# Kernel tuning notes

Measured on AMD Instinct MI355X. Metric: run time of the kernel, lower is better.

The kernel has to match this reference:

```python
import jax, jax.numpy as jnp
import numpy as np

L = 2048          # seq len
DIM = 1024        # model dim
NL = 12           # num layers
VOCAB = 50257
PAD_VOCAB = 50264 # vocab padded to multiple of 8 for embedding
N = 16            # ssm state dim
K = 4             # conv kernel size
E = 2048          # d_inner = expand * dim
DTR = 64          # dt_rank = ceil(dim/16)
EPS = 1e-5


def setup_inputs() -> dict:
    key = jax.random.key(0)
    ks = jax.random.split(key, 12)
    s = 0.02
    f32 = jnp.float32
    # HiPPO-style A init: A_log = log(1..N) broadcast over channels
    A_log = jnp.log(jnp.broadcast_to(jnp.arange(1, N + 1, dtype=f32), (NL, E, N)))
    return {
        "input_ids": jax.random.randint(ks[0], (L,), 0, VOCAB),
        "embed": jax.random.normal(ks[1], (PAD_VOCAB, DIM), f32) * s,
        "in_proj_w": jax.random.normal(ks[2], (NL, 2 * E, DIM), f32) * s,
        "conv_w": jax.random.normal(ks[3], (NL, E, K), f32) * s,
        "conv_b": jnp.zeros((NL, E), f32),
        "x_proj_w": jax.random.normal(ks[4], (NL, DTR + 2 * N, E), f32) * s,
        "dt_proj_w": jax.random.normal(ks[5], (NL, E, DTR), f32) * s,
        "dt_proj_b": jax.random.normal(ks[6], (NL, E), f32) * 0.1,
        "A_log": A_log,
        "D_param": jnp.ones((NL, E), f32),
        "out_proj_w": jax.random.normal(ks[7], (NL, DIM, E), f32) * s,
        "norm_w": jnp.ones((NL, DIM), f32),
        "norm_f_w": jnp.ones((DIM,), f32),
        "head_w": jax.random.normal(ks[8], (VOCAB, DIM), f32) * s,
    }


def rmsnorm(x, w):
    # per-token RMSNorm over last axis (matches eqx.nn.RMSNorm vmapped per token)
    inv = jax.lax.rsqrt(jnp.mean(x * x, axis=-1, keepdims=True) + EPS)
    return x * inv * w


def causal_dw_conv(x, w, b):
    # x: [L, E], w: [E, K] depthwise causal conv, b: [E]
    out = jax.lax.conv_general_dilated(
        x.T[None],            # [1, E, L]
        w[:, None, :],        # [E, 1, K]
        (1,), [(K - 1, 0)],
        feature_group_count=E,
        dimension_numbers=("NCH", "OIH", "NCH"),
    )
    return out[0].T + b       # [L, E]


def mamba_block(x, in_w, cw, cb, xp_w, dt_w, dt_b, A_log, D, out_w):
    # x: [L, DIM]
    xz = x @ in_w.T                       # [L, 2E]
    xi, z = xz[:, :E], xz[:, E:]
    xc = jax.nn.silu(causal_dw_conv(xi, cw, cb))   # [L, E]
    dbc = xc @ xp_w.T                     # [L, DTR + 2N]
    dt = jax.nn.softplus(dbc[:, :DTR] @ dt_w.T + dt_b)  # [L, E]
    B = dbc[:, DTR:DTR + N]               # [L, N]
    C = dbc[:, DTR + N:]                  # [L, N]
    A = -jnp.exp(A_log)                   # [E, N]
    dA = jnp.exp(dt[:, :, None] * A)                       # [L, E, N]
    dBu = dt[:, :, None] * B[:, None, :] * xc[:, :, None]  # [L, E, N]

    def step(h, inp):
        dA_t, dBu_t = inp
        h = dA_t * h + dBu_t
        return h, h

    _, hs = jax.lax.scan(step, jnp.zeros((E, N), x.dtype), (dA, dBu))
    y = jnp.einsum("len,ln->le", hs, C) + D * xc
    y = y * jax.nn.silu(z)
    return y @ out_w.T                    # [L, DIM]


def reference(input_ids, embed, in_proj_w, conv_w, conv_b, x_proj_w,
              dt_proj_w, dt_proj_b, A_log, D_param, out_proj_w,
              norm_w, norm_f_w, head_w):
    x = embed[input_ids]                  # [L, DIM]
    res = None
    for i in range(NL):
        res = x + res if res is not None else x
        h = rmsnorm(res, norm_w[i])
        x = mamba_block(h, in_proj_w[i], conv_w[i], conv_b[i], x_proj_w[i],
                        dt_proj_w[i], dt_proj_b[i], A_log[i], D_param[i],
                        out_proj_w[i])
    res = x + res
    x = rmsnorm(res, norm_f_w)
    return x @ head_w.T                   # [L, VOCAB]
```

## Files before the change

### kernel.cpp

```cpp
#include <hip/hip_runtime.h>
#include <math.h>

#define LSEQ 2048
#define DMODEL 1024
#define NLAYER 12
#define NVOCAB 50257
#define NPADV 50304
#define EDIM 2048
#define NST 16
#define DTRANK 64
#define EPSV 1e-5f
#define NCHUNK 64
#define TCHUNK 32

typedef __attribute__((ext_vector_type(4))) float float4v;
typedef __attribute__((ext_vector_type(8))) short short8v;
typedef __attribute__((ext_vector_type(4))) unsigned short ushort4v;
typedef unsigned short u16;

__device__ __forceinline__ u16 f2bf(float f) {
    union { float f; unsigned int u; } v; v.f = f;
    unsigned int r = v.u + 0x7FFFu + ((v.u >> 16) & 1u);
    return (u16)(r >> 16);
}

__device__ __forceinline__ ushort4v cvt4(float4 a) {
    ushort4v r; r[0] = f2bf(a.x); r[1] = f2bf(a.y); r[2] = f2bf(a.z); r[3] = f2bf(a.w);
    return r;
}

__device__ __forceinline__ float4v mfma_bf16(short8v a, short8v b, float4v c) {
    return __builtin_amdgcn_mfma_f32_16x16x32_bf16(a, b, c, 0, 0, 0);
}

__device__ __forceinline__ void gload_lds16(const void* g, void* l) {
    __builtin_amdgcn_global_load_lds(
        (const __attribute__((address_space(1))) unsigned int*)g,
        (__attribute__((address_space(3))) unsigned int*)l,
        16, 0, 0);
}

__global__ __launch_bounds__(256) void k_embed(const int* __restrict__ ids,
                                               const float* __restrict__ emb,
                                               float* __restrict__ res) {
    const int t = blockIdx.x;
    const int row = ids[t];
    ((float4*)(res + (size_t)t * DMODEL))[threadIdx.x] =
        ((const float4*)(emb + (size_t)row * DMODEL))[threadIdx.x];
}

template<bool ADD>
__global__ __launch_bounds__(256) void k_addnorm(float* __restrict__ res,
                                                 const float* __restrict__ xin,
                                                 const float* __restrict__ w,
                                                 u16* __restrict__ h) {
    const int t = blockIdx.x;
    const int i = threadIdx.x;
    float4 r = ((float4*)(res + (size_t)t * DMODEL))[i];
    if (ADD) {
        float4 xv = ((const float4*)(xin + (size_t)t * DMODEL))[i];
        r.x += xv.x; r.y += xv.y; r.z += xv.z; r.w += xv.w;
        ((float4*)(res + (size_t)t * DMODEL))[i] = r;
    }
    float ss = r.x * r.x + r.y * r.y + r.z * r.z + r.w * r.w;
#pragma unroll
    for (int off = 32; off > 0; off >>= 1) ss += __shfl_xor(ss, off);
    __shared__ float part[4];
    if ((i & 63) == 0) part[i >> 6] = ss;
    __syncthreads();
    float tot = part[0] + part[1] + part[2] + part[3];
    const float inv = rsqrtf(tot * (1.f / DMODEL) + EPSV);
    float4 wv = ((const float4*)w)[i];
    float4 o;
    o.x = r.x * inv * wv.x; o.y = r.y * inv * wv.y;
    o.z = r.z * inv * wv.z; o.w = r.w * inv * wv.w;
    ((ushort4v*)(h + (size_t)t * DMODEL))[i] = cvt4(o);
}

__global__ __launch_bounds__(256) void k_cvt(const float* __restrict__ s, u16* __restrict__ d,
                                             long long n, long long ntot) {
    const long long stride = (long long)gridDim.x * 256 * 8;
    for (long long i = ((long long)blockIdx.x * 256 + threadIdx.x) * 8; i < ntot; i += stride) {
        ushort4v lo, hi;
        if (i < n) {
            float4 a = *(const float4*)(s + i);
            float4 b = *(const float4*)(s + i + 4);
            lo = cvt4(a); hi = cvt4(b);
        } else {
            lo[0] = lo[1] = lo[2] = lo[3] = 0;
            hi[0] = hi[1] = hi[2] = hi[3] = 0;
        }
        *(ushort4v*)(d + i) = lo;
        *(ushort4v*)(d + i + 4) = hi;
    }
}

__global__ __launch_bounds__(256) void k_cvtL(const float* __restrict__ sa, u16* __restrict__ da, long long na,
                                              const float* __restrict__ sb, u16* __restrict__ db, long long nb,
                                              const float* __restrict__ sc, u16* __restrict__ dc, long long nc,
                                              const float* __restrict__ sd, u16* __restrict__ dd, long long nd) {
    const long long tot = na + nb + nc + nd;
    const long long stride = (long long)gridDim.x * 256 * 8;
    for (long long i = ((long long)blockIdx.x * 256 + threadIdx.x) * 8; i < tot; i += stride) {
        const float* s; u16* d; long long o = i;
        if (o < na) { s = sa; d = da; }
        else { o -= na;
            if (o < nb) { s = sb; d = db; }
            else { o -= nb;
                if (o < nc) { s = sc; d = dc; }
                else { o -= nc; s = sd; d = dd; } } }
        float4 a = *(const float4*)(s + o);
        float4 b = *(const float4*)(s + o + 4);
        *(ushort4v*)(d + o) = cvt4(a);
        *(ushort4v*)(d + o + 4) = cvt4(b);
    }
}

template<int MT, int EPI, bool NTS>
__global__ __launch_bounds__(256, 4) void k_gemm128(const u16* __restrict__ A,
                                                    const u16* __restrict__ W,
                                                    float* __restrict__ C,
                                                    const float* __restrict__ bias,
                                                    int N, int K, int ldc, int cpx) {
    __shared__ __align__(128) u16 lds[2][8192];
    const int tid = threadIdx.x;
    const int w = tid >> 6;
    const int lane = tid & 63;
    const int l16 = lane & 15;
    const int quad = lane >> 4;
    const int wm = (w >> 1) * 64;
    const int wn = (w & 1) * 64;
    const int bid = blockIdx.x;
    const int orig = (bid & 7) * cpx + (bid >> 3);
    const int bm = orig & (MT - 1);
    const int bn = orig / MT;
    const int row0 = bm * 128, col0 = bn * 128;

    const int scol = ((lane & 3) ^ ((lane >> 3) & 3)) * 8;
    const int lrow = lane >> 2;
    const u16* sbase[4];
#pragma unroll
    for (int c = 0; c < 4; ++c) {
        const int g = w * 4 + c;
        sbase[c] = (g < 8 ? A + (size_t)(row0 + g * 16 + lrow) * K
                          : W + (size_t)(col0 + (g - 8) * 16 + lrow) * K) + scol;
    }

    const int swz = (quad ^ ((l16 >> 1) & 3)) * 8;
    const int aoff = (wm + l16) * 32 + swz;
    const int boff = 4096 + (wn + l16) * 32 + swz;

    float4v acc[4][4];
#pragma unroll
    for (int i = 0; i < 4; ++i)
#pragma unroll
        for (int j = 0; j < 4; ++j)
#pragma unroll
            for (int r = 0; r < 4; ++r) acc[i][j][r] = 0.f;

    const int NT = K >> 5;

    auto stage_tile = [&](int buf, int t) {
#pragma unroll
        for (int c = 0; c < 4; ++c)
            gload_lds16(sbase[c] + t * 32, &lds[buf][(w * 4 + c) * 512]);
    };

    stage_tile(0, 0);
    stage_tile(1, 1);
    asm volatile("s_waitcnt vmcnt(4)" ::: "memory");
    __builtin_amdgcn_s_barrier();

    for (int n = 0; n < NT; ++n) {
        const u16* Ls = &lds[n & 1][0];
        short8v af[4], bf[4];
#pragma unroll
        for (int ii = 0; ii < 4; ++ii)
            af[ii] = *(const short8v*)&Ls[aoff + ii * 512];
#pragma unroll
        for (int j = 0; j < 4; ++j)
            bf[j] = *(const short8v*)&Ls[boff + j * 512];
        __builtin_amdgcn_s_barrier();
        __builtin_amdgcn_s_setprio(1);
#pragma unroll
        for (int ii = 0; ii < 4; ++ii)
#pragma unroll
            for (int j = 0; j < 4; ++j)
                acc[ii][j] = mfma_bf16(af[ii], bf[j], acc[ii][j]);
        __builtin_amdgcn_s_setprio(0);
        if (n + 2 < NT) {
            stage_tile(n & 1, n + 2);
            asm volatile("s_waitcnt vmcnt(4)" ::: "memory");
        } else if (n < NT - 1) {
            asm volatile("s_waitcnt vmcnt(0)" ::: "memory");
        }
        __builtin_amdgcn_s_barrier();
    }

    float* lt = (float*)(&lds[0][0]) + (size_t)w * 1040;
    const int ecol = col0 + wn + lane;
    float bv = 0.f;
    if (EPI == 1) bv = bias[(ecol < N) ? ecol : 0];
#pragma unroll
    for (int i = 0; i < 4; ++i) {
        __syncthreads();
#pragma unroll
        for (int j = 0; j < 4; ++j)
#pragma unroll
            for (int r = 0; r < 4; ++r)
                lt[(quad * 4 + r) * 65 + j * 16 + l16] = acc[i][j][r];
        __syncthreads();
        if (ecol < N) {
            const int rbase = row0 + wm + i * 16;
#pragma unroll
            for (int t = 0; t < 16; ++t) {
                float v = lt[t * 65 + lane];
                if (EPI == 1) { v += bv; v = (v > 20.f) ? v : log1pf(__expf(v)); }
                float* p = &C[(size_t)(rbase + t) * ldc + ecol];
                if (NTS) __builtin_nontemporal_store(v, p);
                else *p = v;
            }
        }
    }
}

template<int TM, int TN>
__global__ __launch_bounds__(256) void k_gemm_bf(const u16* __restrict__ A,
                                                 const u16* __restrict__ W,
                                                 float* __restrict__ C,
                                                 int N, int K, int ldc) {
    constexpr int NI = TM / 32, NJ = TN / 32, CA = TM / 64, CB = TN / 64;
    __shared__ u16 As[TM * 32];
    __shared__ u16 Bs[TN * 32];
    __shared__ float lt_s[4][16 * 33];
    const int tid = threadIdx.x;
    const int lane = tid & 63;
    const int wave = tid >> 6;
    const int l16 = lane & 15;
    const int quad = lane >> 4;
    const int wm = (wave >> 1) * (TM / 2);
    const int wn = (wave & 1) * (TN / 2);
    const int srow = lane >> 2;
    const int scol = ((lane & 3) ^ ((lane >> 3) & 3)) * 8;
    const int bm = blockIdx.x, bn = blockIdx.y;

    const u16* Ab = A + ((size_t)bm * TM + srow) * K + scol;
    const u16* Wb = W + ((size_t)bn * TN + srow) * K + scol;

    const int qs = (quad ^ ((l16 >> 1) & 3)) * 8;

    float4v acc[NI][NJ];
#pragma unroll
    for (int i = 0; i < NI; ++i)
#pragma unroll
        for (int j = 0; j < NJ; ++j)
#pragma unroll
            for (int r = 0; r < 4; ++r) acc[i][j][r] = 0.f;

    for (int k0 = 0; k0 < K; k0 += 32) {
#pragma unroll
        for (int c = 0; c < CA; ++c) {
            const int chunk = wave * CA + c;
            gload_lds16(Ab + (size_t)chunk * 16 * K + k0, &As[chunk * 512]);
        }
#pragma unroll
        for (int c = 0; c < CB; ++c) {
            const int chunk = wave * CB + c;
            gload_lds16(Wb + (size_t)chunk * 16 * K + k0, &Bs[chunk * 512]);
        }
        __syncthreads();
        short8v af[NI], bfr[NJ];
#pragma unroll
        for (int i = 0; i < NI; ++i)
            af[i] = *(const short8v*)&As[(wm + i * 16 + l16) * 32 + qs];
#pragma unroll
        for (int j = 0; j < NJ; ++j)
            bfr[j] = *(const short8v*)&Bs[(wn + j * 16 + l16) * 32 + qs];
#pragma unroll
        for (int i = 0; i < NI; ++i)
#pragma unroll
            for (int j = 0; j < NJ; ++j)
                acc[i][j] = mfma_bf16(af[i], bfr[j], acc[i][j]);
        __syncthreads();
    }

    float* lt = &lt_s[wave][0];
    const int c32 = lane & 31;
    const int rsub = lane >> 5;
    const int ecol = bn * TN + wn + c32;
#pragma unroll
    for (int i = 0; i < NI; ++i) {
        __syncthreads();
#pragma unroll
        for (int j = 0; j < NJ; ++j)
#pragma unroll
            for (int r = 0; r < 4; ++r)
                lt[(quad * 4 + r) * 33 + j * 16 + l16] = acc[i][j][r];
        __syncthreads();
        if (ecol < N) {
            const int rbase = bm * TM + wm + i * 16;
#pragma unroll
            for (int t = 0; t < 8; ++t)
                C[(size_t)(rbase + 2 * t + rsub) * ldc + ecol] =
                    lt[(2 * t + rsub) * 33 + c32];
        }
    }
}

__global__ __launch_bounds__(256) void k_conv(const float* __restrict__ xz,
                                              const float* __restrict__ cw,
                                              const float* __restrict__ cb,
                                              float* __restrict__ xc,
                                              u16* __restrict__ xc16) {
    const int e = blockIdx.x * 256 + threadIdx.x;
    const int t0 = blockIdx.y * 8;
    const float w0 = cw[e * 4 + 0], w1 = cw[e * 4 + 1], w2 = cw[e * 4 + 2], w3 = cw[e * 4 + 3];
    const float b = cb[e];
    float xm3 = (t0 >= 3) ? xz[(size_t)(t0 - 3) * (2 * EDIM) + e] : 0.f;
    float xm2 = (t0 >= 2) ? xz[(size_t)(t0 - 2) * (2 * EDIM) + e] : 0.f;
    float xm1 = (t0 >= 1) ? xz[(size_t)(t0 - 1) * (2 * EDIM) + e] : 0.f;
#pragma unroll
    for (int s = 0; s < 8; ++s) {
        const int t = t0 + s;
        const float xt = xz[(size_t)t * (2 * EDIM) + e];
        const float v = w0 * xm3 + w1 * xm2 + w2 * xm1 + w3 * xt + b;
        const float sv = v / (1.f + __expf(-v));
        xc[(size_t)t * EDIM + e] = sv;
        xc16[(size_t)t * EDIM + e] = f2bf(sv);
        xm3 = xm2; xm2 = xm1; xm1 = xt;
    }
}

__global__ __launch_bounds__(256) void k_xproj(const u16* __restrict__ xc,
                                               const u16* __restrict__ W,
                                               float* __restrict__ dbc,
                                               u16* __restrict__ dbc16) {
    const int tid = threadIdx.x;
    const int wave = tid >> 6, lane = tid & 63;
    const int l16 = lane & 15, quad = lane >> 4;
    const int m = blockIdx.x * 16 + l16;
    const int kb = wave * (EDIM / 4);
    float4v acc[6];
#pragma unroll
    for (int j = 0; j < 6; ++j)
#pragma unroll
        for (int r = 0; r < 4; ++r) acc[j][r] = 0.f;

    for (int ks = 0; ks < EDIM / 4; ks += 32) {
        const int k = kb + ks + quad * 8;
        const short8v af = *(const short8v*)(xc + (size_t)m * EDIM + k);
#pragma unroll
        for (int j = 0; j < 6; ++j) {
            const short8v bf = *(const short8v*)(W + (size_t)(j * 16 + l16) * EDIM + k);
            acc[j] = mfma_bf16(af, bf, acc[j]);
        }
    }
    __shared__ float red[4][16][96];
#pragma unroll
    for (int j = 0; j < 6; ++j)
#pragma unroll
        for (int r = 0; r < 4; ++r)
            red[wave][quad * 4 + r][j * 16 + l16] = acc[j][r];
    __syncthreads();
    for (int idx = tid; idx < 16 * 96; idx += 256) {
        const int r = idx / 96, c = idx % 96;
        const float s = red[0][r][c] + red[1][r][c] + red[2][r][c] + red[3][r][c];
        const int row = blockIdx.x * 16 + r;
        dbc[(size_t)row * 96 + c] = s;
        if (c < 64) dbc16[(size_t)row * 64 + c] = f2bf(s);
    }
}

__global__ __launch_bounds__(256) void k_scanA(const float* __restrict__ dt,
                                               const float* __restrict__ xc,
                                               const float* __restrict__ dbc,
                                               const float* __restrict__ Al,
                                               float* __restrict__ hpart,
                                               float* __restrict__ sdtb) {
    const int e = blockIdx.y * 256 + threadIdx.x;
    const int c = blockIdx.x;
    float a[NST];
#pragma unroll
    for (int n = 0; n < NST; ++n) a[n] = -__expf(Al[(size_t)e * NST + n]);
    bool fast = true;
#pragma unroll
    for (int n = 0; n < NST; ++n)
        fast = fast && (fabsf(a[n] + (float)(n + 1)) < 1e-3f * (float)(n + 1));
    __align__(16) float h[NST];
#pragma unroll
    for (int n = 0; n < NST; ++n) h[n] = 0.f;
    float sdt = 0.f;
    const int t0 = c * TCHUNK;
    if (fast) {
        for (int s = 0; s < TCHUNK; ++s) {
            const int t = t0 + s;
            const float d = dt[(size_t)t * EDIM + e];
            const float x = xc[(size_t)t * EDIM + e];
            __align__(16) float Bv[NST];
#pragma unroll
            for (int q = 0; q < 4; ++q)
                *(float4*)&Bv[q * 4] = *(const float4*)&dbc[(size_t)t * 96 + 64 + q * 4];
            const float u = d * x;
            sdt += d;
            const float d1 = __expf(-d);
            float pw = 1.f;
#pragma unroll
            for (int n = 0; n < NST; ++n) { pw *= d1; h[n] = fmaf(pw, h[n], u * Bv[n]); }
        }
    } else {
        for (int s = 0; s < TCHUNK; ++s) {
            const int t = t0 + s;
            const float d = dt[(size_t)t * EDIM + e];
            const float x = xc[(size_t)t * EDIM + e];
            __align__(16) float Bv[NST];
#pragma unroll
            for (int q = 0; q < 4; ++q)
                *(float4*)&Bv[q * 4] = *(const float4*)&dbc[(size_t)t * 96 + 64 + q * 4];
            const float u = d * x;
            sdt += d;
#pragma unroll
            for (int n = 0; n < NST; ++n) h[n] = fmaf(__expf(d * a[n]), h[n], u * Bv[n]);
        }
    }
#pragma unroll
    for (int n = 0; n < NST; n += 4)
        *(float4*)&hpart[((size_t)c * EDIM + e) * NST + n] = *(float4*)&h[n];
    sdtb[(size_t)c * EDIM + e] = sdt;
}

__global__ __launch_bounds__(256) void k_scanB(float* __restrict__ hio,
                                               const float* __restrict__ sdtb,
                                               const float* __restrict__ Al) {
    const int idx = blockIdx.x * 256 + threadIdx.x;
    const int e = idx >> 4;
    const float a = -__expf(Al[idx]);
    float carry = 0.f;
    for (int c = 0; c < NCHUNK; ++c) {
        const size_t off = ((size_t)c * EDIM + e) * NST + (idx & 15);
        const float hp = hio[off];
        const float ap = __expf(a * sdtb[(size_t)c * EDIM + e]);
        hio[off] = carry;
        carry = fmaf(ap, carry, hp);
    }
}

__global__ __launch_bounds__(256) void k_scanC(const float* __restrict__ dt,
                                               const float* __restrict__ xc,
                                               const float* __restrict__ dbc,
                                               const float* __restrict__ xz,
                                               const float* __restrict__ Al,
                                               const float* __restrict__ Dl,
                                               const float* __restrict__ hin,
                                               u16* __restrict__ y) {
    const int e = blockIdx.y * 256 + threadIdx.x;
    const int c = blockIdx.x;
    float a[NST];
#pragma unroll
    for (int n = 0; n < NST; ++n) a[n] = -__expf(Al[(size_t)e * NST + n]);
    bool fast = true;
#pragma unroll
    for (int n = 0; n < NST; ++n)
        fast = fast && (fabsf(a[n] + (float)(n + 1)) < 1e-3f * (float)(n + 1));
    __align__(16) float h[NST];
#pragma unroll
    for (int n = 0; n < NST; n += 4)
        *(float4*)&h[n] = *(const float4*)&hin[((size_t)c * EDIM + e) * NST + n];
    const float Dv = Dl[e];
    const int t0 = c * TCHUNK;
    for (int s = 0; s < TCHUNK; ++s) {
        const int t = t0 + s;
        const float d = dt[(size_t)t * EDIM + e];
        const float x = xc[(size_t)t * EDIM + e];
        __align__(16) float Bv[NST], Cv[NST];
#pragma unroll
        for (int q = 0; q < 4; ++q) {
            *(float4*)&Bv[q * 4] = *(const float4*)&dbc[(size_t)t * 96 + 64 + q * 4];
            *(float4*)&Cv[q * 4] = *(const float4*)&dbc[(size_t)t * 96 + 80 + q * 4];
        }
        const float u = d * x;
        float ys = 0.f;
        if (fast) {
            const float d1 = __expf(-d);
            float pw = 1.f;
#pragma unroll
            for (int n = 0; n < NST; ++n) {
                pw *= d1;
                h[n] = fmaf(pw, h[n], u * Bv[n]);
                ys = fmaf(h[n], Cv[n], ys);
            }
        } else {
#pragma unroll
            for (int n = 0; n < NST; ++n) {
                h[n] = fmaf(__expf(d * a[n]), h[n], u * Bv[n]);
                ys = fmaf(h[n], Cv[n], ys);
            }
        }
        const float z = xz[(size_t)t * (2 * EDIM) + EDIM + e];
        const float yv = ys + Dv * x;
        y[(size_t)t * EDIM + e] = f2bf(yv * (z / (1.f + __expf(-z))));
    }
}

extern "C" void kernel_launch(void* const* d_in, const int* in_sizes, int n_in,
                              void* d_out, int out_size, void* d_ws, size_t ws_size,
                              hipStream_t stream) {
    const int*   ids   = (const int*)d_in[0];
    const float* emb   = (const float*)d_in[1];
    const float* inW   = (const float*)d_in[2];
    const float* convW = (const float*)d_in[3];
    const float* convB = (const float*)d_in[4];
    const float* xpW   = (const float*)d_in[5];
    const float* dtW   = (const float*)d_in[6];
    const float* dtB   = (const float*)d_in[7];
    const float* Alog  = (const float*)d_in[8];
    const float* Dpar  = (const float*)d_in[9];
    const float* outW  = (const float*)d_in[10];
    const float* normW = (const float*)d_in[11];
    const float* normF = (const float*)d_in[12];
    const float* headW = (const float*)d_in[13];
    float* out = (float*)d_out;

    float* ws    = (float*)d_ws;
    float* res   = ws;
    float* xzb   = res   + (size_t)LSEQ * DMODEL;
    float* xcb   = xzb   + (size_t)LSEQ * 2 * EDIM;
    float* dbcb  = xcb   + (size_t)LSEQ * EDIM;
    float* dtb   = dbcb  + (size_t)LSEQ * 96;
    float* xob   = dtb   + (size_t)LSEQ * EDIM;
    float* hpart = xob   + (size_t)LSEQ * DMODEL;
    float* sdtb  = hpart + (size_t)NCHUNK * EDIM * NST;
    u16* hbf  = (u16*)(sdtb + (size_t)NCHUNK * EDIM);
    u16* ybf  = hbf  + (size_t)LSEQ * DMODEL;
    u16* wbf  = ybf  + (size_t)LSEQ * EDIM;
    u16* wbf2 = wbf  + (size_t)2 * EDIM * DMODEL;
    u16* xc16  = wbf  + (size_t)12 * 1024 * 1024;
    u16* dbc16 = xc16 + (size_t)LSEQ * EDIM;
    u16* xpw16 = dbc16 + (size_t)LSEQ * DTRANK;
    u16* dtw16 = xpw16 + (size_t)96 * EDIM;

    k_embed<<<LSEQ, 256, 0, stream>>>(ids, emb, res);

    for (int i = 0; i < NLAYER; ++i) {
        if (i == 0)
            k_addnorm<false><<<LSEQ, 256, 0, stream>>>(res, nullptr, normW, hbf);
        else
            k_addnorm<true><<<LSEQ, 256, 0, stream>>>(res, xob, normW + (size_t)i * DMODEL, hbf);

        k_cvtL<<<4096, 256, 0, stream>>>(
            inW  + (size_t)i * 2 * EDIM * DMODEL, wbf,   (long long)2 * EDIM * DMODEL,
            outW + (size_t)i * DMODEL * EDIM,     wbf2,  (long long)DMODEL * EDIM,
            xpW  + (size_t)i * 96 * EDIM,         xpw16, (long long)96 * EDIM,
            dtW  + (size_t)i * EDIM * DTRANK,     dtw16, (long long)EDIM * DTRANK);

        k_gemm128<16, 0, false><<<dim3(512), 256, 0, stream>>>(hbf, wbf, xzb, nullptr,
                2 * EDIM, DMODEL, 2 * EDIM, 64);

        k_conv<<<dim3(8, 256), 256, 0, stream>>>(xzb, convW + (size_t)i * EDIM * 4,
                convB + (size_t)i * EDIM, xcb, xc16);

        k_xproj<<<128, 256, 0, stream>>>(xc16, xpw16, dbcb, dbc16);

        k_gemm128<16, 1, false><<<dim3(256), 256, 0, stream>>>(dbc16, dtw16, dtb,
                dtB + (size_t)i * EDIM, EDIM, DTRANK, EDIM, 32);

        const float* Al = Alog + (size_t)i * EDIM * NST;
        k_scanA<<<dim3(NCHUNK, EDIM / 256), 256, 0, stream>>>(dtb, xcb, dbcb, Al, hpart, sdtb);
        k_scanB<<<(EDIM * NST) / 256, 256, 0, stream>>>(hpart, sdtb, Al);
        k_scanC<<<dim3(NCHUNK, EDIM / 256), 256, 0, stream>>>(dtb, xcb, dbcb, xzb, Al,
                Dpar + (size_t)i * EDIM, hpart, ybf);

        k_gemm_bf<64, 64><<<dim3(32, 16), 256, 0, stream>>>(ybf, wbf2, xob,
                DMODEL, EDIM, DMODEL);
    }

    k_addnorm<true><<<LSEQ, 256, 0, stream>>>(res, xob, normF, hbf);

    k_cvt<<<4096, 256, 0, stream>>>(headW, wbf,
            (long long)NVOCAB * DMODEL, (long long)NPADV * DMODEL);
    k_gemm128<16, 0, true><<<dim3(6288), 256, 0, stream>>>(hbf, wbf, out, nullptr,
            NVOCAB, DMODEL, NVOCAB, 6288 / 8);
}
```

Measured before the change: 2.981 ms.

## Triple-buffer LDS in 128-tile GEMM and pipeline out_proj with 64-tile kernel

```diff
diff --git a/kernel.cpp b/kernel.cpp
--- a/kernel.cpp
+++ b/kernel.cpp
@@ -117,12 +117,12 @@
 }
 
 template<int MT, int EPI, bool NTS>
-__global__ __launch_bounds__(256, 4) void k_gemm128(const u16* __restrict__ A,
+__global__ __launch_bounds__(256, 3) void k_gemm128(const u16* __restrict__ A,
                                                     const u16* __restrict__ W,
                                                     float* __restrict__ C,
                                                     const float* __restrict__ bias,
                                                     int N, int K, int ldc, int cpx) {
-    __shared__ __align__(128) u16 lds[2][8192];
+    __shared__ __align__(128) u16 lds[3][8192];
     const int tid = threadIdx.x;
     const int w = tid >> 6;
     const int lane = tid & 63;
@@ -159,11 +159,13 @@
             for (int r = 0; r < 4; ++r) acc[i][j][r] = 0.f;
 
     const int NT = K >> 5;
+    u16* lds0 = &lds[0][0];
 
     auto stage_tile = [&](int buf, int t) {
+        u16* dst = lds0 + buf * 8192;
 #pragma unroll
         for (int c = 0; c < 4; ++c)
-            gload_lds16(sbase[c] + t * 32, &lds[buf][(w * 4 + c) * 512]);
+            gload_lds16(sbase[c] + t * 32, dst + (w * 4 + c) * 512);
     };
 
     stage_tile(0, 0);
@@ -171,8 +173,9 @@
     asm volatile("s_waitcnt vmcnt(4)" ::: "memory");
     __builtin_amdgcn_s_barrier();
 
+    int cur = 0;
     for (int n = 0; n < NT; ++n) {
-        const u16* Ls = &lds[n & 1][0];
+        const u16* Ls = lds0 + cur * 8192;
         short8v af[4], bf[4];
 #pragma unroll
         for (int ii = 0; ii < 4; ++ii)
@@ -180,7 +183,11 @@
 #pragma unroll
         for (int j = 0; j < 4; ++j)
             bf[j] = *(const short8v*)&Ls[boff + j * 512];
-        __builtin_amdgcn_s_barrier();
+        const bool pf = (n + 2 < NT);
+        if (pf) {
+            int tg = cur + 2; if (tg >= 3) tg -= 3;
+            stage_tile(tg, n + 2);
+        }
         __builtin_amdgcn_s_setprio(1);
 #pragma unroll
         for (int ii = 0; ii < 4; ++ii)
@@ -188,16 +195,15 @@
             for (int j = 0; j < 4; ++j)
                 acc[ii][j] = mfma_bf16(af[ii], bf[j], acc[ii][j]);
         __builtin_amdgcn_s_setprio(0);
-        if (n + 2 < NT) {
-            stage_tile(n & 1, n + 2);
+        if (pf)
             asm volatile("s_waitcnt vmcnt(4)" ::: "memory");
-        } else if (n < NT - 1) {
+        else if (n + 1 < NT)
             asm volatile("s_waitcnt vmcnt(0)" ::: "memory");
-        }
         __builtin_amdgcn_s_barrier();
-    }
-
-    float* lt = (float*)(&lds[0][0]) + (size_t)w * 1040;
+        ++cur; if (cur == 3) cur = 0;
+    }
+
+    float* lt = (float*)lds0 + (size_t)w * 1040;
     const int ecol = col0 + wn + lane;
     float bv = 0.f;
     if (EPI == 1) bv = bias[(ecol < N) ? ecol : 0];
@@ -224,81 +230,116 @@
     }
 }
 
-template<int TM, int TN>
-__global__ __launch_bounds__(256) void k_gemm_bf(const u16* __restrict__ A,
-                                                 const u16* __restrict__ W,
-                                                 float* __restrict__ C,
-                                                 int N, int K, int ldc) {
-    constexpr int NI = TM / 32, NJ = TN / 32, CA = TM / 64, CB = TN / 64;
-    __shared__ u16 As[TM * 32];
-    __shared__ u16 Bs[TN * 32];
-    __shared__ float lt_s[4][16 * 33];
+template<int MT>
+__global__ __launch_bounds__(256, 3) void k_gemm64(const u16* __restrict__ A,
+                                                   const u16* __restrict__ W,
+                                                   float* __restrict__ C,
+                                                   int N, int K, int ldc, int cpx) {
+    __shared__ __align__(128) u16 lds[3][8192];
     const int tid = threadIdx.x;
+    const int w = tid >> 6;
     const int lane = tid & 63;
-    const int wave = tid >> 6;
     const int l16 = lane & 15;
     const int quad = lane >> 4;
-    const int wm = (wave >> 1) * (TM / 2);
-    const int wn = (wave & 1) * (TN / 2);
-    const int srow = lane >> 2;
+    const int wm = (w >> 1) * 32;
+    const int wn = (w & 1) * 32;
+    const int bid = blockIdx.x;
+    const int orig = (bid & 7) * cpx + (bid >> 3);
+    const int bm = orig & (MT - 1);
+    const int bn = orig / MT;
+    const int row0 = bm * 64, col0 = bn * 64;
+
     const int scol = ((lane & 3) ^ ((lane >> 3) & 3)) * 8;
-    const int bm = blockIdx.x, bn = blockIdx.y;
-
-    const u16* Ab = A + ((size_t)bm * TM + srow) * K + scol;
-    const u16* Wb = W + ((size_t)bn * TN + srow) * K + scol;
-
-    const int qs = (quad ^ ((l16 >> 1) & 3)) * 8;
-
-    float4v acc[NI][NJ];
-#pragma unroll
-    for (int i = 0; i < NI; ++i)
-#pragma unroll
-        for (int j = 0; j < NJ; ++j)
+    const int lrow = lane >> 2;
+    const u16* sbase[4];
+#pragma unroll
+    for (int c = 0; c < 4; ++c) {
+        const int ch = w * 4 + c;
+        const int isA = (ch < 8);
+        const int cc = isA ? ch : (ch - 8);
+        const int half = cc >> 2;
+        const int rbase = (cc & 3) * 16;
+        sbase[c] = (isA ? A + (size_t)(row0 + rbase + lrow) * K
+                        : W + (size_t)(col0 + rbase + lrow) * K) + half * 32 + scol;
+    }
+
+    const int swz = (quad ^ ((l16 >> 1) & 3)) * 8;
+    const int aoff = (wm + l16) * 32 + swz;
+    const int boff = 4096 + (wn + l16) * 32 + swz;
+
+    float4v acc[2][2];
+#pragma unroll
+    for (int i = 0; i < 2; ++i)
+#pragma unroll
+        for (int j = 0; j < 2; ++j)
 #pragma unroll
             for (int r = 0; r < 4; ++r) acc[i][j][r] = 0.f;
 
-    for (int k0 = 0; k0 < K; k0 += 32) {
-#pragma unroll
-        for (int c = 0; c < CA; ++c) {
-            const int chunk = wave * CA + c;
-            gload_lds16(Ab + (size_t)chunk * 16 * K + k0, &As[chunk * 512]);
-        }
-#pragma unroll
-        for (int c = 0; c < CB; ++c) {
-            const int chunk = wave * CB + c;
-            gload_lds16(Wb + (size_t)chunk * 16 * K + k0, &Bs[chunk * 512]);
-        }
-        __syncthreads();
-        short8v af[NI], bfr[NJ];
-#pragma unroll
-        for (int i = 0; i < NI; ++i)
-            af[i] = *(const short8v*)&As[(wm + i * 16 + l16) * 32 + qs];
-#pragma unroll
-        for (int j = 0; j < NJ; ++j)
-            bfr[j] = *(const short8v*)&Bs[(wn + j * 16 + l16) * 32 + qs];
-#pragma unroll
-        for (int i = 0; i < NI; ++i)
-#pragma unroll
-            for (int j = 0; j < NJ; ++j)
-                acc[i][j] = mfma_bf16(af[i], bfr[j], acc[i][j]);
-        __syncthreads();
-    }
-
-    float* lt = &lt_s[wave][0];
+    const int NT = K >> 6;
+    u16* lds0 = &lds[0][0];
+
+    auto stage_tile = [&](int buf, int t) {
+        u16* dst = lds0 + buf * 8192;
+#pragma unroll
+        for (int c = 0; c < 4; ++c)
+            gload_lds16(sbase[c] + t * 64, dst + (w * 4 + c) * 512);
+    };
+
+    stage_tile(0, 0);
+    stage_tile(1, 1);
+    asm volatile("s_waitcnt vmcnt(4)" ::: "memory");
+    __builtin_amdgcn_s_barrier();
+
+    int cur = 0;
+    for (int n = 0; n < NT; ++n) {
+        const u16* Ls = lds0 + cur * 8192;
+        short8v af[2][2], bf[2][2];
+#pragma unroll
+        for (int ks = 0; ks < 2; ++ks) {
+#pragma unroll
+            for (int ii = 0; ii < 2; ++ii)
+                af[ks][ii] = *(const short8v*)&Ls[ks * 2048 + aoff + ii * 512];
+#pragma unroll
+            for (int j = 0; j < 2; ++j)
+                bf[ks][j] = *(const short8v*)&Ls[ks * 2048 + boff + j * 512];
+        }
+        const bool pf = (n + 2 < NT);
+        if (pf) {
+            int tg = cur + 2; if (tg >= 3) tg -= 3;
+            stage_tile(tg, n + 2);
+        }
+        __builtin_amdgcn_s_setprio(1);
+#pragma unroll
+        for (int ks = 0; ks < 2; ++ks)
+#pragma unroll
+            for (int ii = 0; ii < 2; ++ii)
+#pragma unroll
+                for (int j = 0; j < 2; ++j)
+                    acc[ii][j] = mfma_bf16(af[ks][ii], bf[ks][j], acc[ii][j]);
+        __builtin_amdgcn_s_setprio(0);
+        if (pf)
+            asm volatile("s_waitcnt vmcnt(4)" ::: "memory");
+        else if (n + 1 < NT)
+            asm volatile("s_waitcnt vmcnt(0)" ::: "memory");
+        __builtin_amdgcn_s_barrier();
+        ++cur; if (cur == 3) cur = 0;
+    }
+
+    float* lt = (float*)lds0 + (size_t)w * 528;
     const int c32 = lane & 31;
     const int rsub = lane >> 5;
-    const int ecol = bn * TN + wn + c32;
-#pragma unroll
-    for (int i = 0; i < NI; ++i) {
+    const int ecol = col0 + wn + c32;
+#pragma unroll
+    for (int i = 0; i < 2; ++i) {
         __syncthreads();
 #pragma unroll
-        for (int j = 0; j < NJ; ++j)
+        for (int j = 0; j < 2; ++j)
 #pragma unroll
             for (int r = 0; r < 4; ++r)
                 lt[(quad * 4 + r) * 33 + j * 16 + l16] = acc[i][j][r];
         __syncthreads();
         if (ecol < N) {
-            const int rbase = bm * TM + wm + i * 16;
+            const int rbase = row0 + wm + i * 16;
 #pragma unroll
             for (int t = 0; t < 8; ++t)
                 C[(size_t)(rbase + 2 * t + rsub) * ldc + ecol] =
@@ -569,8 +610,8 @@
         k_scanC<<<dim3(NCHUNK, EDIM / 256), 256, 0, stream>>>(dtb, xcb, dbcb, xzb, Al,
                 Dpar + (size_t)i * EDIM, hpart, ybf);
 
-        k_gemm_bf<64, 64><<<dim3(32, 16), 256, 0, stream>>>(ybf, wbf2, xob,
-                DMODEL, EDIM, DMODEL);
+        k_gemm64<32><<<dim3(512), 256, 0, stream>>>(ybf, wbf2, xob,
+                DMODEL, EDIM, DMODEL, 64);
     }
 
     k_addnorm<true><<<LSEQ, 256, 0, stream>>>(res, xob, normF, hbf);
```

Result: faster. 2.883 ms (-3.3%).
